# Performance work log

Hardware: AMD Instinct MI355X
Metric: run time of the kernel (lower is better)

## Reference

```python
import jax, jax.numpy as jnp
import numpy as np

N_STEP = 3

def setup_inputs() -> dict:
    key = jax.random.key(0)
    ks = jax.random.split(key, 5)
    bs, l, d = 16, 128, 256
    feat = jax.random.normal(ks[0], (bs, l, d), dtype=jnp.float32)
    mask = jnp.ones((bs, l), dtype=jnp.float32)
    # torch nn.Linear init scale ~ 1/sqrt(fan_in)
    agg_w = jax.random.normal(ks[1], (d, d), dtype=jnp.float32) / np.sqrt(d)
    agg_b = jnp.zeros((d,), dtype=jnp.float32)
    attn_w = jax.random.normal(ks[2], (d, 2 * d), dtype=jnp.float32) / np.sqrt(2 * d)
    attn_b = jnp.zeros((d,), dtype=jnp.float32)
    upd_w = jax.random.normal(ks[3], (d, 2 * d), dtype=jnp.float32) / np.sqrt(2 * d)
    upd_b = jnp.zeros((d,), dtype=jnp.float32)
    return {"feat": feat, "mask": mask, "agg_w": agg_w, "agg_b": agg_b,
            "attn_w": attn_w, "attn_b": attn_b, "upd_w": upd_w, "upd_b": upd_b}


def reference(feat, mask, agg_w, agg_b, attn_w, attn_b, upd_w, upd_b):
    # Faithful, vectorized version of GCNShared.forward (eval mode: dropout = identity).
    # attn(cat(xhid_i, xhid_j)) splits into xhid_i @ W1.T + xhid_j @ W2.T + b.
    bs, l, d = feat.shape
    W1 = attn_w[:, :d]   # acts on xhid (the full sequence, index i)
    W2 = attn_w[:, d:]   # acts on the broadcast query token j
    hid = feat
    for _ in range(N_STEP):
        hid = hid * mask[:, :, None]
        xhid = jnp.einsum('bid,ed->bie', hid, agg_w) + agg_b  # [bs, l, d]
        s1 = jnp.einsum('bid,ed->bie', xhid, W1)  # key-side term,  [bs, i, d]
        s2 = jnp.einsum('bjd,ed->bje', xhid, W2)  # query-side term, [bs, j, d]
        # scores[b, j, i, e]: per-feature pairwise attention logits
        scores = s1[:, None, :, :] + s2[:, :, None, :] + attn_b
        w = jax.nn.softmax(scores, axis=2)  # softmax over sequence dim i (dim=1 in torch)
        agg = jax.nn.sigmoid(jnp.einsum('bjie,bie->bje', w, xhid))  # [bs, l, d]
        xcat = jnp.concatenate([xhid, agg], axis=2)  # [bs, l, 2d]
        hid = jnp.einsum('bjf,ef->bje', xcat, upd_w) + upd_b
    return hid
```

## Files before the change

kernel.cpp:

```cpp
#include <hip/hip_runtime.h>
#include <cmath>


#define FMA16(av,bv,acc)                                                        \
  acc[0][0]=fmaf(av.x,bv.x,acc[0][0]); acc[0][1]=fmaf(av.x,bv.y,acc[0][1]);     \
  acc[0][2]=fmaf(av.x,bv.z,acc[0][2]); acc[0][3]=fmaf(av.x,bv.w,acc[0][3]);     \
  acc[1][0]=fmaf(av.y,bv.x,acc[1][0]); acc[1][1]=fmaf(av.y,bv.y,acc[1][1]);     \
  acc[1][2]=fmaf(av.y,bv.z,acc[1][2]); acc[1][3]=fmaf(av.y,bv.w,acc[1][3]);     \
  acc[2][0]=fmaf(av.z,bv.x,acc[2][0]); acc[2][1]=fmaf(av.z,bv.y,acc[2][1]);     \
  acc[2][2]=fmaf(av.z,bv.z,acc[2][2]); acc[2][3]=fmaf(av.z,bv.w,acc[2][3]);     \
  acc[3][0]=fmaf(av.w,bv.x,acc[3][0]); acc[3][1]=fmaf(av.w,bv.y,acc[3][1]);     \
  acc[3][2]=fmaf(av.w,bv.z,acc[3][2]); acc[3][3]=fmaf(av.w,bv.w,acc[3][3]);

template<int AMODE>
__device__ __forceinline__ void gemm64(
    const float* __restrict__ Asrc, const float* __restrict__ Wt, int wld, int c0,
    int r0, const float* __restrict__ maskp, const float* abL,
    const float* caL, float* As, float* Bs, int t, float (&acc)[4][4])
{
    const int tx = t & 15, ty = t >> 4;
    const int ar = t >> 3, ak = (t & 7) << 2;
    const int bk = t >> 4, bc4 = (t & 15) << 2;
    float4 va0, va1, vb0, vb1;

    va0 = *(const float4*)(Asrc + (size_t)(r0 + ar) * 256 + ak);
    va1 = *(const float4*)(Asrc + (size_t)(r0 + ar + 32) * 256 + ak);
    vb0 = *(const float4*)(Wt + (size_t)bk * wld + c0 + bc4);
    vb1 = *(const float4*)(Wt + (size_t)(bk + 16) * wld + c0 + bc4);

    for (int ch = 0; ch < 8; ++ch) {
        const int k0 = ch * 32;
        {
            float4 v = va0;
            if (AMODE == 2) {
                const float mv = maskp[r0 + ar];
                float4 c4 = *(const float4*)(caL + k0 + ak);
                float4 b4 = *(const float4*)(abL + k0 + ak);
                v.x = fmaf(mv, v.x + c4.x, b4.x); v.y = fmaf(mv, v.y + c4.y, b4.y);
                v.z = fmaf(mv, v.z + c4.z, b4.z); v.w = fmaf(mv, v.w + c4.w, b4.w);
            }
            As[(ak + 0) * 68 + ar] = v.x; As[(ak + 1) * 68 + ar] = v.y;
            As[(ak + 2) * 68 + ar] = v.z; As[(ak + 3) * 68 + ar] = v.w;
            v = va1;
            if (AMODE == 2) {
                const float mv = maskp[r0 + ar + 32];
                float4 c4 = *(const float4*)(caL + k0 + ak);
                float4 b4 = *(const float4*)(abL + k0 + ak);
                v.x = fmaf(mv, v.x + c4.x, b4.x); v.y = fmaf(mv, v.y + c4.y, b4.y);
                v.z = fmaf(mv, v.z + c4.z, b4.z); v.w = fmaf(mv, v.w + c4.w, b4.w);
            }
            As[(ak + 0) * 68 + ar + 32] = v.x; As[(ak + 1) * 68 + ar + 32] = v.y;
            As[(ak + 2) * 68 + ar + 32] = v.z; As[(ak + 3) * 68 + ar + 32] = v.w;
            *(float4*)&Bs[bk * 68 + bc4] = vb0;
            *(float4*)&Bs[(bk + 16) * 68 + bc4] = vb1;
        }
        __syncthreads();
        if (ch < 7) {
            const int kn = k0 + 32;
            va0 = *(const float4*)(Asrc + (size_t)(r0 + ar) * 256 + kn + ak);
            va1 = *(const float4*)(Asrc + (size_t)(r0 + ar + 32) * 256 + kn + ak);
            vb0 = *(const float4*)(Wt + (size_t)(kn + bk) * wld + c0 + bc4);
            vb1 = *(const float4*)(Wt + (size_t)(kn + bk + 16) * wld + c0 + bc4);
        }
        #pragma unroll
        for (int kk = 0; kk < 32; ++kk) {
            float4 av = *(const float4*)&As[kk * 68 + ty * 4];
            float4 bv = *(const float4*)&Bs[kk * 68 + tx * 4];
            FMA16(av, bv, acc)
        }
        __syncthreads();
    }
}

template<int AMODE>
__device__ __forceinline__ void stats_epi(
    const float* __restrict__ Asrc, const float* __restrict__ maskp,
    const float* abL, const float* caL,
    int r0, int c0, int bx, int t, const float (&acc)[4][4],
    float* __restrict__ pz, float* __restrict__ pa)
{
    const int tx = t & 15, ty = t >> 4;
    const int e = c0 + tx * 4;
    float xh[4][4];
    #pragma unroll
    for (int i = 0; i < 4; ++i) {
        const int r = r0 + ty * 4 + i;
        float4 v = *(const float4*)(Asrc + (size_t)r * 256 + e);
        if (AMODE == 2) {
            const float mv = maskp[r];
            float4 c4 = *(const float4*)(caL + e);
            float4 b4 = *(const float4*)(abL + e);
            v.x = fmaf(mv, v.x + c4.x, b4.x); v.y = fmaf(mv, v.y + c4.y, b4.y);
            v.z = fmaf(mv, v.z + c4.z, b4.z); v.w = fmaf(mv, v.w + c4.w, b4.w);
        }
        xh[i][0] = v.x; xh[i][1] = v.y; xh[i][2] = v.z; xh[i][3] = v.w;
    }
    float pzv[4], pav[4];
    #pragma unroll
    for (int j = 0; j < 4; ++j) {
        float p0 = __expf(acc[0][j]), p1 = __expf(acc[1][j]);
        float p2 = __expf(acc[2][j]), p3 = __expf(acc[3][j]);
        pzv[j] = (p0 + p1) + (p2 + p3);
        pav[j] = fmaf(p0, xh[0][j], fmaf(p1, xh[1][j], fmaf(p2, xh[2][j], p3 * xh[3][j])));
    }
    const int gg = bx * 16 + ty;
    *(float4*)(pz + (size_t)gg * 256 + e) = make_float4(pzv[0], pzv[1], pzv[2], pzv[3]);
    *(float4*)(pa + (size_t)gg * 256 + e) = make_float4(pav[0], pav[1], pav[2], pav[3]);
}

__device__ __forceinline__ void write_epi(float* __restrict__ dst, int r0, int c0,
                                          int t, const float (&acc)[4][4]) {
    const int tx = t & 15, ty = t >> 4;
    const int e = c0 + tx * 4;
    #pragma unroll
    for (int i = 0; i < 4; ++i)
        *(float4*)(dst + (size_t)(r0 + ty * 4 + i) * 256 + e) =
            make_float4(acc[i][0], acc[i][1], acc[i][2], acc[i][3]);
}

__device__ inline void transp(const float* __restrict__ src, int sld, int scol0,
                              float* __restrict__ dst, int dld,
                              int ti, int tt, float* lds) {
    const int tr = (ti >> 3) * 32, tc = (ti & 7) * 32;
    const int rr = tt >> 5, cc = tt & 31;
    #pragma unroll
    for (int p = 0; p < 4; ++p) {
        int row = p * 8 + rr;
        lds[row * 33 + cc] = src[(size_t)(tr + row) * sld + scol0 + tc + cc];
    }
    __syncthreads();
    #pragma unroll
    for (int p = 0; p < 4; ++p) {
        int krow = p * 8 + rr;
        dst[(size_t)(tc + krow) * dld + tr + cc] = lds[cc * 33 + krow];
    }
    __syncthreads();
}

__global__ __launch_bounds__(256) void l0_k(
    const float* __restrict__ feat, const float* __restrict__ mask,
    const float* __restrict__ agg_w, const float* __restrict__ agg_b,
    const float* __restrict__ attn_w, const float* __restrict__ upd_w,
    const float* __restrict__ upd_b,
    float* __restrict__ wt12, float* __restrict__ u1t, float* __restrict__ u2t,
    float* __restrict__ m2t, float* __restrict__ v0, float* __restrict__ buf0)
{
    const int bid = blockIdx.x, t = threadIdx.x;
    __shared__ __align__(16) float shb[4352];

    if (bid < 128) {
        const int co = (bid < 64) ? 0 : 256;
        const int e0 = (bid & 63) * 4;
        float (&agL)[4][256] = *(float (*)[4][256])shb;
        {
            int row = t >> 6, d0 = (t & 63) * 4;
            *(float4*)&agL[row][d0] = *(const float4*)(agg_w + (size_t)(e0 + row) * 256 + d0);
        }
        __syncthreads();
        float acc[4] = {0.f, 0.f, 0.f, 0.f};
        #pragma unroll 4
        for (int d = 0; d < 256; ++d) {
            float u = upd_w[(size_t)d * 512 + co + t];
            acc[0] = fmaf(agL[0][d], u, acc[0]);
            acc[1] = fmaf(agL[1][d], u, acc[1]);
            acc[2] = fmaf(agL[2][d], u, acc[2]);
            acc[3] = fmaf(agL[3][d], u, acc[3]);
        }
        if (bid < 64) {
            #pragma unroll
            for (int i = 0; i < 4; ++i)
                wt12[(size_t)t * 512 + 256 + e0 + i] = acc[i];
        } else {
            #pragma unroll
            for (int i = 0; i < 4; ++i)
                m2t[(size_t)t * 256 + e0 + i] = acc[i];
        }
    } else if (bid < 192) {
        transp(attn_w, 512, 0, wt12, 512, bid - 128, t, shb);
    } else if (bid < 256) {
        transp(upd_w, 512, 0, u1t, 256, bid - 192, t, shb);
    } else if (bid < 320) {
        transp(upd_w, 512, 256, u2t, 256, bid - 256, t, shb);
    } else if (bid == 320) {
        float* ub = shb;
        ub[t] = upd_b[t];
        __syncthreads();
        float acc = 0.f;
        const float* wr = agg_w + (size_t)t * 256;
        #pragma unroll 8
        for (int d = 0; d < 256; ++d) acc = fmaf(wr[d], ub[d], acc);
        v0[t] = acc;
    } else {
        const int v = bid - 321;
        const int r0 = (v & 31) * 64, e0 = (v >> 5) * 64;
        float* As = shb; float* Bs = shb + 2176;
        const int tx = t & 15, ty = t >> 4;
        const int ar = t >> 3, ak = (t & 7) << 2;
        float acc[4][4] = {};
        for (int k0 = 0; k0 < 256; k0 += 32) {
            #pragma unroll
            for (int h = 0; h < 2; ++h) {
                const int row = ar + 32 * h;
                float4 va = *(const float4*)(feat + (size_t)(r0 + row) * 256 + k0 + ak);
                const float mv = mask[r0 + row];
                As[(ak + 0) * 68 + row] = va.x * mv; As[(ak + 1) * 68 + row] = va.y * mv;
                As[(ak + 2) * 68 + row] = va.z * mv; As[(ak + 3) * 68 + row] = va.w * mv;
                float4 vb = *(const float4*)(agg_w + (size_t)(e0 + row) * 256 + k0 + ak);
                Bs[(ak + 0) * 68 + row] = vb.x; Bs[(ak + 1) * 68 + row] = vb.y;
                Bs[(ak + 2) * 68 + row] = vb.z; Bs[(ak + 3) * 68 + row] = vb.w;
            }
            __syncthreads();
            #pragma unroll
            for (int kk = 0; kk < 32; ++kk) {
                float4 av = *(const float4*)&As[kk * 68 + ty * 4];
                float4 bv = *(const float4*)&Bs[kk * 68 + tx * 4];
                FMA16(av, bv, acc)
            }
            __syncthreads();
        }
        const int e = e0 + tx * 4;
        float4 b4 = *(const float4*)(agg_b + e);
        #pragma unroll
        for (int i = 0; i < 4; ++i)
            *(float4*)(buf0 + (size_t)(r0 + ty * 4 + i) * 256 + e) =
                make_float4(acc[i][0] + b4.x, acc[i][1] + b4.y,
                            acc[i][2] + b4.z, acc[i][3] + b4.w);
    }
}

__global__ __launch_bounds__(256) void big1_k(
    const float* __restrict__ buf0, const float* __restrict__ wt12,
    float* __restrict__ kst, float* __restrict__ buf1,
    float* __restrict__ pz0, float* __restrict__ pa0)
{
    __shared__ __align__(16) float shb[4352];
    const int t = threadIdx.x;
    const int bx = blockIdx.x, by = blockIdx.y;

    if (bx >= 32) {
        const int k0 = ((bx - 32) * 8 + by) * 4;
        float (&agL)[4][256] = *(float (*)[4][256])shb;
        {
            int row = t >> 6, d0 = (t & 63) * 4;
            *(float4*)&agL[row][d0] =
                *(const float4*)(wt12 + (size_t)(k0 + row) * 512 + 256 + d0);
        }
        __syncthreads();
        float acc[4] = {0.f, 0.f, 0.f, 0.f};
        #pragma unroll 4
        for (int d = 0; d < 256; ++d) {
            float w = wt12[(size_t)d * 512 + t];
            acc[0] = fmaf(agL[0][d], w, acc[0]);
            acc[1] = fmaf(agL[1][d], w, acc[1]);
            acc[2] = fmaf(agL[2][d], w, acc[2]);
            acc[3] = fmaf(agL[3][d], w, acc[3]);
        }
        #pragma unroll
        for (int i = 0; i < 4; ++i)
            kst[(size_t)(k0 + i) * 256 + t] = acc[i];
        return;
    }

    float* As = shb; float* Bs = shb + 2176;
    const int r0 = bx * 64;
    const int c0 = (by < 4) ? by * 64 : 256 + (by - 4) * 64;
    float acc[4][4] = {};
    gemm64<0>(buf0, wt12, 512, c0, r0, nullptr, nullptr, nullptr, As, Bs, t, acc);
    if (by < 4)
        stats_epi<0>(buf0, nullptr, nullptr, nullptr, r0, c0, bx, t, acc, pz0, pa0);
    else
        write_epi(buf1, r0, c0 - 256, t, acc);
}

__global__ __launch_bounds__(1024) void ck1_k(
    const float* __restrict__ pz0, const float* __restrict__ pa0,
    const float* __restrict__ m2t, const float* __restrict__ v0,
    float* __restrict__ caG)
{
    __shared__ float zr[4][256], arr[4][256], aggL[256];
    const int tid = threadIdx.x, t = tid & 255, s = tid >> 8;
    const int b = blockIdx.x;
    float z = 0.f, a = 0.f;
    #pragma unroll
    for (int g = 8 * s; g < 8 * s + 8; ++g) {
        size_t idx = (size_t)(b * 32 + g) * 256 + t;
        z += pz0[idx]; a += pa0[idx];
    }
    zr[s][t] = z; arr[s][t] = a;
    __syncthreads();
    if (s == 0) {
        z = (zr[0][t] + zr[1][t]) + (zr[2][t] + zr[3][t]);
        a = (arr[0][t] + arr[1][t]) + (arr[2][t] + arr[3][t]);
        aggL[t] = 1.f / (1.f + __expf(-(a / z)));
    }
    __syncthreads();
    float ca = 0.f;
    #pragma unroll 8
    for (int d = 64 * s; d < 64 * s + 64; ++d)
        ca = fmaf(aggL[d], m2t[(size_t)d * 256 + t], ca);
    zr[s][t] = ca;
    __syncthreads();
    if (s == 0)
        caG[b * 256 + t] = v0[t] + (zr[0][t] + zr[1][t]) + (zr[2][t] + zr[3][t]);
}

__global__ __launch_bounds__(256) void big2_k(
    const float* __restrict__ buf1, const float* __restrict__ wt12,
    const float* __restrict__ kst, const float* __restrict__ caG,
    const float* __restrict__ mask, const float* __restrict__ agg_b,
    float* __restrict__ buf0, float* __restrict__ buf2,
    float* __restrict__ pz1, float* __restrict__ pa1)
{
    __shared__ __align__(16) float shb[4864];
    float* As = shb; float* Bs = shb + 2176;
    float* caL = shb + 4352; float* abL = shb + 4608;

    const int t = threadIdx.x;
    const int bx = blockIdx.x, by = blockIdx.y;
    const int r0 = bx * 64, b = bx >> 1;

    caL[t] = caG[b * 256 + t];
    abL[t] = agg_b[t];
    __syncthreads();

    float acc[4][4] = {};
    if (by < 4) {
        const int c0 = by * 64;
        gemm64<2>(buf1, wt12, 512, c0, r0, mask, abL, caL, As, Bs, t, acc);
        stats_epi<2>(buf1, mask, abL, caL, r0, c0, bx, t, acc, pz1, pa1);
    } else if (by < 8) {
        const int c0 = 256 + (by - 4) * 64;
        gemm64<2>(buf1, wt12, 512, c0, r0, mask, abL, caL, As, Bs, t, acc);
        write_epi(buf0, r0, c0 - 256, t, acc);
    } else {
        const int c0 = (by - 8) * 64;
        gemm64<2>(buf1, kst, 256, c0, r0, mask, abL, caL, As, Bs, t, acc);
        write_epi(buf2, r0, c0, t, acc);
    }
}

__global__ __launch_bounds__(1024) void ck2_k(
    const float* __restrict__ pz1, const float* __restrict__ pa1,
    const float* __restrict__ g2, const float* __restrict__ s3,
    const float* __restrict__ m2t, const float* __restrict__ u2t,
    const float* __restrict__ v0, const float* __restrict__ agg_b,
    const float* __restrict__ upd_b,
    float* __restrict__ caG2, float* __restrict__ c3G)
{
    __shared__ float zr[4][256], arr[4][256], aggL[256], caL[256], a3L[256];
    const int tid = threadIdx.x, t = tid & 255, s = tid >> 8;
    const int b = blockIdx.x;

    float z = 0.f, a = 0.f;
    #pragma unroll
    for (int g = 8 * s; g < 8 * s + 8; ++g) {
        size_t idx = (size_t)(b * 32 + g) * 256 + t;
        z += pz1[idx]; a += pa1[idx];
    }
    zr[s][t] = z; arr[s][t] = a;
    __syncthreads();
    if (s == 0) {
        z = (zr[0][t] + zr[1][t]) + (zr[2][t] + zr[3][t]);
        a = (arr[0][t] + arr[1][t]) + (arr[2][t] + arr[3][t]);
        aggL[t] = 1.f / (1.f + __expf(-(a / z)));
    }
    __syncthreads();
    float ca = 0.f;
    #pragma unroll 8
    for (int d = 64 * s; d < 64 * s + 64; ++d)
        ca = fmaf(aggL[d], m2t[(size_t)d * 256 + t], ca);
    zr[s][t] = ca;
    __syncthreads();
    if (s == 0) {
        float c = v0[t] + (zr[0][t] + zr[1][t]) + (zr[2][t] + zr[3][t]);
        caL[t] = c;
        caG2[b * 256 + t] = c;
    }
    __syncthreads();
    float z2 = 0.f, a2 = 0.f;
    const size_t rb = (size_t)b * 128;
    #pragma unroll 4
    for (int r = 32 * s; r < 32 * s + 32; ++r) {
        float p = __expf(s3[(rb + r) * 256 + t]);
        z2 += p;
        a2 = fmaf(p, g2[(rb + r) * 256 + t], a2);
    }
    zr[s][t] = z2; arr[s][t] = a2;
    __syncthreads();
    if (s == 0) {
        z2 = (zr[0][t] + zr[1][t]) + (zr[2][t] + zr[3][t]);
        a2 = (arr[0][t] + arr[1][t]) + (arr[2][t] + arr[3][t]);
        float A3 = a2 / z2 + caL[t] + agg_b[t];
        a3L[t] = 1.f / (1.f + __expf(-A3));
    }
    __syncthreads();
    float c3 = 0.f;
    #pragma unroll 8
    for (int d = 64 * s; d < 64 * s + 64; ++d)
        c3 = fmaf(a3L[d], u2t[(size_t)d * 256 + t], c3);
    zr[s][t] = c3;
    __syncthreads();
    if (s == 0)
        c3G[b * 256 + t] = upd_b[t] + (zr[0][t] + zr[1][t]) + (zr[2][t] + zr[3][t]);
}

__global__ __launch_bounds__(256) void big3_k(
    const float* __restrict__ buf0, const float* __restrict__ u1t,
    const float* __restrict__ caG2, const float* __restrict__ c3G,
    const float* __restrict__ mask, const float* __restrict__ agg_b,
    float* __restrict__ outp)
{
    __shared__ __align__(16) float shb[3840];
    float* As2 = shb;
    float* Bs  = shb + 1152;
    float* caL = shb + 3328;
    float* abL = shb + 3584;

    const int t = threadIdx.x;
    const int bx = blockIdx.x, by = blockIdx.y;
    const int r0 = bx * 32, b = bx >> 2;
    const int c0 = by * 64;

    caL[t] = caG2[b * 256 + t];
    abL[t] = agg_b[t];
    __syncthreads();

    const int tx = t & 15, ty = t >> 4;
    const int ar = t >> 3, ak = (t & 7) << 2;
    const int bk = t >> 4, bc4 = (t & 15) << 2;
    float acc[2][4] = {};
    float4 va, vb0, vb1;
    va  = *(const float4*)(buf0 + (size_t)(r0 + ar) * 256 + ak);
    vb0 = *(const float4*)(u1t + (size_t)bk * 256 + c0 + bc4);
    vb1 = *(const float4*)(u1t + (size_t)(bk + 16) * 256 + c0 + bc4);

    for (int ch = 0; ch < 8; ++ch) {
        const int k0 = ch * 32;
        {
            float4 v = va;
            const float mv = mask[r0 + ar];
            float4 c4 = *(const float4*)(caL + k0 + ak);
            float4 b4 = *(const float4*)(abL + k0 + ak);
            v.x = fmaf(mv, v.x + c4.x, b4.x); v.y = fmaf(mv, v.y + c4.y, b4.y);
            v.z = fmaf(mv, v.z + c4.z, b4.z); v.w = fmaf(mv, v.w + c4.w, b4.w);
            As2[(ak + 0) * 36 + ar] = v.x; As2[(ak + 1) * 36 + ar] = v.y;
            As2[(ak + 2) * 36 + ar] = v.z; As2[(ak + 3) * 36 + ar] = v.w;
            *(float4*)&Bs[bk * 68 + bc4] = vb0;
            *(float4*)&Bs[(bk + 16) * 68 + bc4] = vb1;
        }
        __syncthreads();
        if (ch < 7) {
            const int kn = k0 + 32;
            va  = *(const float4*)(buf0 + (size_t)(r0 + ar) * 256 + kn + ak);
            vb0 = *(const float4*)(u1t + (size_t)(kn + bk) * 256 + c0 + bc4);
            vb1 = *(const float4*)(u1t + (size_t)(kn + bk + 16) * 256 + c0 + bc4);
        }
        #pragma unroll
        for (int kk = 0; kk < 32; ++kk) {
            float2 a2v = *(const float2*)&As2[kk * 36 + ty * 2];
            float4 bv  = *(const float4*)&Bs[kk * 68 + tx * 4];
            acc[0][0]=fmaf(a2v.x,bv.x,acc[0][0]); acc[0][1]=fmaf(a2v.x,bv.y,acc[0][1]);
            acc[0][2]=fmaf(a2v.x,bv.z,acc[0][2]); acc[0][3]=fmaf(a2v.x,bv.w,acc[0][3]);
            acc[1][0]=fmaf(a2v.y,bv.x,acc[1][0]); acc[1][1]=fmaf(a2v.y,bv.y,acc[1][1]);
            acc[1][2]=fmaf(a2v.y,bv.z,acc[1][2]); acc[1][3]=fmaf(a2v.y,bv.w,acc[1][3]);
        }
        __syncthreads();
    }
    const int e = c0 + tx * 4;
    float4 cc = *(const float4*)(c3G + b * 256 + e);
    #pragma unroll
    for (int i = 0; i < 2; ++i)
        *(float4*)(outp + (size_t)(r0 + ty * 2 + i) * 256 + e) =
            make_float4(acc[i][0] + cc.x, acc[i][1] + cc.y,
                        acc[i][2] + cc.z, acc[i][3] + cc.w);
}

extern "C" void kernel_launch(void* const* d_in, const int* in_sizes, int n_in,
                              void* d_out, int out_size, void* d_ws, size_t ws_size,
                              hipStream_t stream) {
    const float* feat   = (const float*)d_in[0];
    const float* mask   = (const float*)d_in[1];
    const float* agg_w  = (const float*)d_in[2];
    const float* agg_b  = (const float*)d_in[3];
    const float* attn_w = (const float*)d_in[4];
    const float* upd_w  = (const float*)d_in[6];
    const float* upd_b  = (const float*)d_in[7];
    float* out = (float*)d_out;

    float* p    = (float*)d_ws;
    float* wt12 = p; p += 256 * 512;
    float* u1t  = p; p += 256 * 256;
    float* u2t  = p; p += 256 * 256;
    float* m2t  = p; p += 256 * 256;
    float* kst  = p; p += 256 * 256;
    float* v0   = p; p += 256;
    float* buf0 = p; p += 2048 * 256;
    float* buf1 = p; p += 2048 * 256;
    float* buf2 = p; p += 2048 * 256;
    float* pz0  = p; p += 512 * 256;
    float* pa0  = p; p += 512 * 256;
    float* pz1  = p; p += 512 * 256;
    float* pa1  = p; p += 512 * 256;
    float* caG  = p; p += 16 * 256;
    float* caG2 = p; p += 16 * 256;
    float* c3G  = p; p += 16 * 256;

    l0_k<<<449, 256, 0, stream>>>(feat, mask, agg_w, agg_b, attn_w, upd_w, upd_b,
                                  wt12, u1t, u2t, m2t, v0, buf0);
    big1_k<<<dim3(40, 8), 256, 0, stream>>>(buf0, wt12, kst, buf1, pz0, pa0);
    ck1_k<<<16, 1024, 0, stream>>>(pz0, pa0, m2t, v0, caG);
    big2_k<<<dim3(32, 12), 256, 0, stream>>>(buf1, wt12, kst, caG, mask, agg_b,
                                             buf0, buf2, pz1, pa1);
    ck2_k<<<16, 1024, 0, stream>>>(pz1, pa1, buf0, buf2, m2t, u2t, v0, agg_b, upd_b,
                                   caG2, c3G);
    big3_k<<<dim3(64, 4), 256, 0, stream>>>(buf0, u1t, caG2, c3G, mask, agg_b, out);
}
```

Measured before the change: 84.97 us.

## Use 64-deep K chunks in shared GEMM and tile weight-product precomputes

The shared 64x64 GEMM helper now loads 64-wide K chunks (4 iterations instead of 8), which halves the number of barriers but doubles LDS per block. The weight-fusion precomputes (agg_w·upd_w and the kst product) move from per-thread scalar dot loops onto the tiled GEMM with a transposed epilogue, and this reduces their block counts. big3 switches from 32-row to 64-row tiles with 4x4 accumulators. Occupancy may drop because of the larger shared memory footprint, and big3 now launches fewer blocks.

```diff
diff --git a/kernel.cpp b/kernel.cpp
--- a/kernel.cpp
+++ b/kernel.cpp
@@ -13,57 +13,53 @@
   acc[3][2]=fmaf(av.w,bv.z,acc[3][2]); acc[3][3]=fmaf(av.w,bv.w,acc[3][3]);
 
 template<int AMODE>
-__device__ __forceinline__ void gemm64(
-    const float* __restrict__ Asrc, const float* __restrict__ Wt, int wld, int c0,
-    int r0, const float* __restrict__ maskp, const float* abL,
-    const float* caL, float* As, float* Bs, int t, float (&acc)[4][4])
+__device__ __forceinline__ void gemm64c(
+    const float* __restrict__ Asrc, int astride, int aoff,
+    const float* __restrict__ Wt, int wld, int c0,
+    int r0, const float* __restrict__ maskp,
+    const float* abL, const float* caL,
+    float* As, float* Bs, int t, float (&acc)[4][4])
 {
     const int tx = t & 15, ty = t >> 4;
-    const int ar = t >> 3, ak = (t & 7) << 2;
-    const int bk = t >> 4, bc4 = (t & 15) << 2;
-    float4 va0, va1, vb0, vb1;
-
-    va0 = *(const float4*)(Asrc + (size_t)(r0 + ar) * 256 + ak);
-    va1 = *(const float4*)(Asrc + (size_t)(r0 + ar + 32) * 256 + ak);
-    vb0 = *(const float4*)(Wt + (size_t)bk * wld + c0 + bc4);
-    vb1 = *(const float4*)(Wt + (size_t)(bk + 16) * wld + c0 + bc4);
-
-    for (int ch = 0; ch < 8; ++ch) {
-        const int k0 = ch * 32;
-        {
-            float4 v = va0;
-            if (AMODE == 2) {
-                const float mv = maskp[r0 + ar];
-                float4 c4 = *(const float4*)(caL + k0 + ak);
-                float4 b4 = *(const float4*)(abL + k0 + ak);
+    const int arow = t >> 2, s16 = (t & 3) * 16;
+    const float mv = (AMODE != 0) ? maskp[r0 + arow] : 1.f;
+    const float* ap = Asrc + (size_t)(r0 + arow) * astride + aoff + s16;
+    const float* bp = Wt + (size_t)arow * wld + c0 + s16;
+
+    float4 pa[4], pb[4];
+    #pragma unroll
+    for (int i = 0; i < 4; ++i) {
+        pa[i] = *(const float4*)(ap + 4 * i);
+        pb[i] = *(const float4*)(bp + 4 * i);
+    }
+
+    for (int ch = 0; ch < 4; ++ch) {
+        const int k0 = ch * 64;
+        #pragma unroll
+        for (int i = 0; i < 4; ++i) {
+            float4 v = pa[i];
+            if (AMODE == 1) { v.x *= mv; v.y *= mv; v.z *= mv; v.w *= mv; }
+            else if (AMODE == 2) {
+                float4 c4 = *(const float4*)(caL + k0 + s16 + 4 * i);
+                float4 b4 = *(const float4*)(abL + k0 + s16 + 4 * i);
                 v.x = fmaf(mv, v.x + c4.x, b4.x); v.y = fmaf(mv, v.y + c4.y, b4.y);
                 v.z = fmaf(mv, v.z + c4.z, b4.z); v.w = fmaf(mv, v.w + c4.w, b4.w);
             }
-            As[(ak + 0) * 68 + ar] = v.x; As[(ak + 1) * 68 + ar] = v.y;
-            As[(ak + 2) * 68 + ar] = v.z; As[(ak + 3) * 68 + ar] = v.w;
-            v = va1;
-            if (AMODE == 2) {
-                const float mv = maskp[r0 + ar + 32];
-                float4 c4 = *(const float4*)(caL + k0 + ak);
-                float4 b4 = *(const float4*)(abL + k0 + ak);
-                v.x = fmaf(mv, v.x + c4.x, b4.x); v.y = fmaf(mv, v.y + c4.y, b4.y);
-                v.z = fmaf(mv, v.z + c4.z, b4.z); v.w = fmaf(mv, v.w + c4.w, b4.w);
-            }
-            As[(ak + 0) * 68 + ar + 32] = v.x; As[(ak + 1) * 68 + ar + 32] = v.y;
-            As[(ak + 2) * 68 + ar + 32] = v.z; As[(ak + 3) * 68 + ar + 32] = v.w;
-            *(float4*)&Bs[bk * 68 + bc4] = vb0;
-            *(float4*)&Bs[(bk + 16) * 68 + bc4] = vb1;
+            const int kb = s16 + 4 * i;
+            As[(kb + 0) * 68 + arow] = v.x; As[(kb + 1) * 68 + arow] = v.y;
+            As[(kb + 2) * 68 + arow] = v.z; As[(kb + 3) * 68 + arow] = v.w;
+            *(float4*)&Bs[arow * 68 + s16 + 4 * i] = pb[i];
         }
         __syncthreads();
-        if (ch < 7) {
-            const int kn = k0 + 32;
-            va0 = *(const float4*)(Asrc + (size_t)(r0 + ar) * 256 + kn + ak);
-            va1 = *(const float4*)(Asrc + (size_t)(r0 + ar + 32) * 256 + kn + ak);
-            vb0 = *(const float4*)(Wt + (size_t)(kn + bk) * wld + c0 + bc4);
-            vb1 = *(const float4*)(Wt + (size_t)(kn + bk + 16) * wld + c0 + bc4);
+        if (ch < 3) {
+            #pragma unroll
+            for (int i = 0; i < 4; ++i) {
+                pa[i] = *(const float4*)(ap + (ch + 1) * 64 + 4 * i);
+                pb[i] = *(const float4*)(bp + (size_t)(ch + 1) * 64 * wld + 4 * i);
+            }
         }
         #pragma unroll
-        for (int kk = 0; kk < 32; ++kk) {
+        for (int kk = 0; kk < 64; ++kk) {
             float4 av = *(const float4*)&As[kk * 68 + ty * 4];
             float4 bv = *(const float4*)&Bs[kk * 68 + tx * 4];
             FMA16(av, bv, acc)
@@ -118,6 +114,16 @@
             make_float4(acc[i][0], acc[i][1], acc[i][2], acc[i][3]);
 }
 
+__device__ __forceinline__ void write_epiT(float* __restrict__ dst, int ld, int off,
+                                           int r0, int k0, int t, const float (&acc)[4][4]) {
+    const int tx = t & 15, ty = t >> 4;
+    #pragma unroll
+    for (int j = 0; j < 4; ++j) {
+        float4 v = make_float4(acc[0][j], acc[1][j], acc[2][j], acc[3][j]);
+        *(float4*)(dst + (size_t)(k0 + tx * 4 + j) * ld + off + r0 + ty * 4) = v;
+    }
+}
+
 __device__ inline void transp(const float* __restrict__ src, int sld, int scol0,
                               float* __restrict__ dst, int dld,
                               int ti, int tt, float* lds) {
@@ -146,42 +152,24 @@
     float* __restrict__ m2t, float* __restrict__ v0, float* __restrict__ buf0)
 {
     const int bid = blockIdx.x, t = threadIdx.x;
-    __shared__ __align__(16) float shb[4352];
-
-    if (bid < 128) {
-        const int co = (bid < 64) ? 0 : 256;
-        const int e0 = (bid & 63) * 4;
-        float (&agL)[4][256] = *(float (*)[4][256])shb;
-        {
-            int row = t >> 6, d0 = (t & 63) * 4;
-            *(float4*)&agL[row][d0] = *(const float4*)(agg_w + (size_t)(e0 + row) * 256 + d0);
-        }
-        __syncthreads();
-        float acc[4] = {0.f, 0.f, 0.f, 0.f};
-        #pragma unroll 4
-        for (int d = 0; d < 256; ++d) {
-            float u = upd_w[(size_t)d * 512 + co + t];
-            acc[0] = fmaf(agL[0][d], u, acc[0]);
-            acc[1] = fmaf(agL[1][d], u, acc[1]);
-            acc[2] = fmaf(agL[2][d], u, acc[2]);
-            acc[3] = fmaf(agL[3][d], u, acc[3]);
-        }
-        if (bid < 64) {
-            #pragma unroll
-            for (int i = 0; i < 4; ++i)
-                wt12[(size_t)t * 512 + 256 + e0 + i] = acc[i];
-        } else {
-            #pragma unroll
-            for (int i = 0; i < 4; ++i)
-                m2t[(size_t)t * 256 + e0 + i] = acc[i];
-        }
-    } else if (bid < 192) {
-        transp(attn_w, 512, 0, wt12, 512, bid - 128, t, shb);
-    } else if (bid < 256) {
-        transp(upd_w, 512, 0, u1t, 256, bid - 192, t, shb);
-    } else if (bid < 320) {
-        transp(upd_w, 512, 256, u2t, 256, bid - 256, t, shb);
-    } else if (bid == 320) {
+    __shared__ __align__(16) float shb[8704];
+
+    if (bid < 32) {
+        const int idx = bid & 15;
+        const int er = (idx >> 2) * 64, kc = (idx & 3) * 64;
+        const int co = (bid < 16) ? 0 : 256;
+        float acc[4][4] = {};
+        gemm64c<0>(agg_w, 256, 0, upd_w, 512, co + kc, er, nullptr, nullptr, nullptr,
+                   shb, shb + 4352, t, acc);
+        if (bid < 16) write_epiT(wt12, 512, 256, er, kc, t, acc);
+        else          write_epiT(m2t,  256, 0,   er, kc, t, acc);
+    } else if (bid < 96) {
+        transp(attn_w, 512, 0, wt12, 512, bid - 32, t, shb);
+    } else if (bid < 160) {
+        transp(upd_w, 512, 0, u1t, 256, bid - 96, t, shb);
+    } else if (bid < 224) {
+        transp(upd_w, 512, 256, u2t, 256, bid - 160, t, shb);
+    } else if (bid == 224) {
         float* ub = shb;
         ub[t] = upd_b[t];
         __syncthreads();
@@ -191,7 +179,7 @@
         for (int d = 0; d < 256; ++d) acc = fmaf(wr[d], ub[d], acc);
         v0[t] = acc;
     } else {
-        const int v = bid - 321;
+        const int v = bid - 225;
         const int r0 = (v & 31) * 64, e0 = (v >> 5) * 64;
         float* As = shb; float* Bs = shb + 2176;
         const int tx = t & 15, ty = t >> 4;
@@ -233,39 +221,26 @@
     float* __restrict__ kst, float* __restrict__ buf1,
     float* __restrict__ pz0, float* __restrict__ pa0)
 {
-    __shared__ __align__(16) float shb[4352];
+    __shared__ __align__(16) float shb[8704];
     const int t = threadIdx.x;
     const int bx = blockIdx.x, by = blockIdx.y;
 
     if (bx >= 32) {
-        const int k0 = ((bx - 32) * 8 + by) * 4;
-        float (&agL)[4][256] = *(float (*)[4][256])shb;
-        {
-            int row = t >> 6, d0 = (t & 63) * 4;
-            *(float4*)&agL[row][d0] =
-                *(const float4*)(wt12 + (size_t)(k0 + row) * 512 + 256 + d0);
-        }
-        __syncthreads();
-        float acc[4] = {0.f, 0.f, 0.f, 0.f};
-        #pragma unroll 4
-        for (int d = 0; d < 256; ++d) {
-            float w = wt12[(size_t)d * 512 + t];
-            acc[0] = fmaf(agL[0][d], w, acc[0]);
-            acc[1] = fmaf(agL[1][d], w, acc[1]);
-            acc[2] = fmaf(agL[2][d], w, acc[2]);
-            acc[3] = fmaf(agL[3][d], w, acc[3]);
-        }
-        #pragma unroll
-        for (int i = 0; i < 4; ++i)
-            kst[(size_t)(k0 + i) * 256 + t] = acc[i];
+        const int idx = (bx - 32) * 8 + by;
+        if (idx >= 16) return;
+        const int kr = (idx >> 2) * 64, ec = (idx & 3) * 64;
+        float acc[4][4] = {};
+        gemm64c<0>(wt12, 512, 256, wt12, 512, ec, kr, nullptr, nullptr, nullptr,
+                   shb, shb + 4352, t, acc);
+        write_epi(kst, kr, ec, t, acc);
         return;
     }
 
-    float* As = shb; float* Bs = shb + 2176;
     const int r0 = bx * 64;
     const int c0 = (by < 4) ? by * 64 : 256 + (by - 4) * 64;
     float acc[4][4] = {};
-    gemm64<0>(buf0, wt12, 512, c0, r0, nullptr, nullptr, nullptr, As, Bs, t, acc);
+    gemm64c<0>(buf0, 256, 0, wt12, 512, c0, r0, nullptr, nullptr, nullptr,
+               shb, shb + 4352, t, acc);
     if (by < 4)
         stats_epi<0>(buf0, nullptr, nullptr, nullptr, r0, c0, bx, t, acc, pz0, pa0);
     else
@@ -311,9 +286,9 @@
     float* __restrict__ buf0, float* __restrict__ buf2,
     float* __restrict__ pz1, float* __restrict__ pa1)
 {
-    __shared__ __align__(16) float shb[4864];
-    float* As = shb; float* Bs = shb + 2176;
-    float* caL = shb + 4352; float* abL = shb + 4608;
+    __shared__ __align__(16) float shb[9216];
+    float* As = shb; float* Bs = shb + 4352;
+    float* caL = shb + 8704; float* abL = shb + 8960;
 
     const int t = threadIdx.x;
     const int bx = blockIdx.x, by = blockIdx.y;
@@ -326,15 +301,15 @@
     float acc[4][4] = {};
     if (by < 4) {
         const int c0 = by * 64;
-        gemm64<2>(buf1, wt12, 512, c0, r0, mask, abL, caL, As, Bs, t, acc);
+        gemm64c<2>(buf1, 256, 0, wt12, 512, c0, r0, mask, abL, caL, As, Bs, t, acc);
         stats_epi<2>(buf1, mask, abL, caL, r0, c0, bx, t, acc, pz1, pa1);
     } else if (by < 8) {
         const int c0 = 256 + (by - 4) * 64;
-        gemm64<2>(buf1, wt12, 512, c0, r0, mask, abL, caL, As, Bs, t, acc);
+        gemm64c<2>(buf1, 256, 0, wt12, 512, c0, r0, mask, abL, caL, As, Bs, t, acc);
         write_epi(buf0, r0, c0 - 256, t, acc);
     } else {
         const int c0 = (by - 8) * 64;
-        gemm64<2>(buf1, kst, 256, c0, r0, mask, abL, caL, As, Bs, t, acc);
+        gemm64c<2>(buf1, 256, 0, kst, 256, c0, r0, mask, abL, caL, As, Bs, t, acc);
         write_epi(buf2, r0, c0, t, acc);
     }
 }
@@ -410,67 +385,28 @@
     const float* __restrict__ mask, const float* __restrict__ agg_b,
     float* __restrict__ outp)
 {
-    __shared__ __align__(16) float shb[3840];
-    float* As2 = shb;
-    float* Bs  = shb + 1152;
-    float* caL = shb + 3328;
-    float* abL = shb + 3584;
+    __shared__ __align__(16) float shb[9216];
+    float* As = shb; float* Bs = shb + 4352;
+    float* caL = shb + 8704; float* abL = shb + 8960;
 
     const int t = threadIdx.x;
     const int bx = blockIdx.x, by = blockIdx.y;
-    const int r0 = bx * 32, b = bx >> 2;
+    const int r0 = bx * 64, b = bx >> 1;
     const int c0 = by * 64;
 
     caL[t] = caG2[b * 256 + t];
     abL[t] = agg_b[t];
     __syncthreads();
 
+    float acc[4][4] = {};
+    gemm64c<2>(buf0, 256, 0, u1t, 256, c0, r0, mask, abL, caL, As, Bs, t, acc);
+
     const int tx = t & 15, ty = t >> 4;
-    const int ar = t >> 3, ak = (t & 7) << 2;
-    const int bk = t >> 4, bc4 = (t & 15) << 2;
-    float acc[2][4] = {};
-    float4 va, vb0, vb1;
-    va  = *(const float4*)(buf0 + (size_t)(r0 + ar) * 256 + ak);
-    vb0 = *(const float4*)(u1t + (size_t)bk * 256 + c0 + bc4);
-    vb1 = *(const float4*)(u1t + (size_t)(bk + 16) * 256 + c0 + bc4);
-
-    for (int ch = 0; ch < 8; ++ch) {
-        const int k0 = ch * 32;
-        {
-            float4 v = va;
-            const float mv = mask[r0 + ar];
-            float4 c4 = *(const float4*)(caL + k0 + ak);
-            float4 b4 = *(const float4*)(abL + k0 + ak);
-            v.x = fmaf(mv, v.x + c4.x, b4.x); v.y = fmaf(mv, v.y + c4.y, b4.y);
-            v.z = fmaf(mv, v.z + c4.z, b4.z); v.w = fmaf(mv, v.w + c4.w, b4.w);
-            As2[(ak + 0) * 36 + ar] = v.x; As2[(ak + 1) * 36 + ar] = v.y;
-            As2[(ak + 2) * 36 + ar] = v.z; As2[(ak + 3) * 36 + ar] = v.w;
-            *(float4*)&Bs[bk * 68 + bc4] = vb0;
-            *(float4*)&Bs[(bk + 16) * 68 + bc4] = vb1;
-        }
-        __syncthreads();
-        if (ch < 7) {
-            const int kn = k0 + 32;
-            va  = *(const float4*)(buf0 + (size_t)(r0 + ar) * 256 + kn + ak);
-            vb0 = *(const float4*)(u1t + (size_t)(kn + bk) * 256 + c0 + bc4);
-            vb1 = *(const float4*)(u1t + (size_t)(kn + bk + 16) * 256 + c0 + bc4);
-        }
-        #pragma unroll
-        for (int kk = 0; kk < 32; ++kk) {
-            float2 a2v = *(const float2*)&As2[kk * 36 + ty * 2];
-            float4 bv  = *(const float4*)&Bs[kk * 68 + tx * 4];
-            acc[0][0]=fmaf(a2v.x,bv.x,acc[0][0]); acc[0][1]=fmaf(a2v.x,bv.y,acc[0][1]);
-            acc[0][2]=fmaf(a2v.x,bv.z,acc[0][2]); acc[0][3]=fmaf(a2v.x,bv.w,acc[0][3]);
-            acc[1][0]=fmaf(a2v.y,bv.x,acc[1][0]); acc[1][1]=fmaf(a2v.y,bv.y,acc[1][1]);
-            acc[1][2]=fmaf(a2v.y,bv.z,acc[1][2]); acc[1][3]=fmaf(a2v.y,bv.w,acc[1][3]);
-        }
-        __syncthreads();
-    }
     const int e = c0 + tx * 4;
     float4 cc = *(const float4*)(c3G + b * 256 + e);
     #pragma unroll
-    for (int i = 0; i < 2; ++i)
-        *(float4*)(outp + (size_t)(r0 + ty * 2 + i) * 256 + e) =
+    for (int i = 0; i < 4; ++i)
+        *(float4*)(outp + (size_t)(r0 + ty * 4 + i) * 256 + e) =
             make_float4(acc[i][0] + cc.x, acc[i][1] + cc.y,
                         acc[i][2] + cc.z, acc[i][3] + cc.w);
 }
@@ -505,13 +441,13 @@
     float* caG2 = p; p += 16 * 256;
     float* c3G  = p; p += 16 * 256;
 
-    l0_k<<<449, 256, 0, stream>>>(feat, mask, agg_w, agg_b, attn_w, upd_w, upd_b,
+    l0_k<<<353, 256, 0, stream>>>(feat, mask, agg_w, agg_b, attn_w, upd_w, upd_b,
                                   wt12, u1t, u2t, m2t, v0, buf0);
-    big1_k<<<dim3(40, 8), 256, 0, stream>>>(buf0, wt12, kst, buf1, pz0, pa0);
+    big1_k<<<dim3(34, 8), 256, 0, stream>>>(buf0, wt12, kst, buf1, pz0, pa0);
     ck1_k<<<16, 1024, 0, stream>>>(pz0, pa0, m2t, v0, caG);
     big2_k<<<dim3(32, 12), 256, 0, stream>>>(buf1, wt12, kst, caG, mask, agg_b,
                                              buf0, buf2, pz1, pa1);
     ck2_k<<<16, 1024, 0, stream>>>(pz1, pa1, buf0, buf2, m2t, u2t, v0, agg_b, upd_b,
                                    caG2, c3G);
-    big3_k<<<dim3(64, 4), 256, 0, stream>>>(buf0, u1t, caG2, c3G, mask, agg_b, out);
-}
+    big3_k<<<dim3(32, 4), 256, 0, stream>>>(buf0, u1t, caG2, c3G, mask, agg_b, out);
+}
```

New measurement: 113.7 us. 33.8% more time.
